# Kernel tuning notes

Hardware: AMD Instinct MI355X
Metric: run time of the kernel (lower is better)

Reference implementation:

```python
import jax, jax.numpy as jnp
import numpy as np

N, E, B = 20000, 320000, 64
HID, DEPTH, NFREQ = 128, 4, 8
NODE_DIM, EDGE_DIM, SG = 4, 3, 230
TWO_PI = 2.0 * np.pi


def setup_inputs() -> dict:
    key = jax.random.key(0)
    ks = jax.random.split(key, 20)
    inp = {}
    inp["x"] = jax.random.normal(ks[0], (N, NODE_DIM), jnp.float32)
    inp["edge_index"] = jax.random.randint(ks[1], (2, E), 0, N)
    inp["edge_attr"] = jax.random.normal(ks[2], (E, EDGE_DIM), jnp.float32)
    inp["batch"] = jnp.sort(jax.random.randint(ks[3], (N,), 0, B))
    inp["space_group"] = jax.random.randint(ks[4], (B,), 0, SG)
    inp["node_w"] = jax.random.normal(ks[5], (NODE_DIM, HID), jnp.float32) * 0.1
    inp["node_b"] = jnp.zeros((HID,), jnp.float32)
    inp["sg_table"] = jax.random.normal(ks[6], (SG, HID), jnp.float32) * 0.1
    inp["lin_w"] = jax.random.normal(ks[7], (DEPTH, 2 * HID + EDGE_DIM, HID), jnp.float32) * 0.05
    inp["lin_b"] = jnp.zeros((DEPTH, HID), jnp.float32)
    inp["att_w"] = jax.random.normal(ks[8], (DEPTH, 2 * HID + EDGE_DIM), jnp.float32) * 0.05
    inp["att_b"] = jnp.zeros((DEPTH,), jnp.float32)
    inp["fk_w"] = jax.random.normal(ks[9], (DEPTH, NFREQ, HID, HID), jnp.float32) * 0.1
    inp["fk_b"] = jnp.zeros((DEPTH, HID), jnp.float32)
    inp["bn_g"] = jnp.ones((DEPTH, HID), jnp.float32)
    inp["bn_b"] = jnp.zeros((DEPTH, HID), jnp.float32)
    inp["pool_w"] = jax.random.normal(ks[10], (HID,), jnp.float32) * 0.1
    inp["pool_b"] = jnp.zeros((), jnp.float32)
    inp["head_w1"] = jax.random.normal(ks[11], (4, 2 * HID, HID), jnp.float32) * 0.05
    inp["head_b1"] = jnp.zeros((4, HID), jnp.float32)
    for i, (nm, od) in enumerate([("e", 1), ("s", 3), ("c", 7), ("m", 3)]):
        inp[nm + "_w2"] = jax.random.normal(ks[12 + i], (HID, od), jnp.float32) * 0.05
        inp[nm + "_b2"] = jnp.zeros((od,), jnp.float32)
    return inp


def reference(x, edge_index, edge_attr, batch, space_group, node_w, node_b, sg_table,
              lin_w, lin_b, att_w, att_b, fk_w, fk_b, bn_g, bn_b, pool_w, pool_b,
              head_w1, head_b1, e_w2, e_b2, s_w2, s_b2, c_w2, c_b2, m_w2, m_b2):
    src, dst = edge_index[0], edge_index[1]  # x_j = x[src], x_i = x[dst]
    h = x @ node_w + node_b                  # [N, HID]
    sg = sg_table[space_group]               # [B, HID]
    freqs = jnp.arange(1, NFREQ + 1, dtype=h.dtype)
    for l in range(DEPTH):
        # edge conv: gather-concat-linear-sigmoid attention-scatter add
        tmp = jnp.concatenate([h[dst], h[src], edge_attr], axis=-1)   # [E, 2H+3]
        alpha = jax.nn.sigmoid(tmp @ att_w[l] + att_b[l])[:, None]    # [E, 1]
        msg = alpha * (tmp @ lin_w[l] + lin_b[l])                     # [E, H]
        h_conv = jax.ops.segment_sum(msg, dst, num_segments=N)
        # Fourier-Kolmogorov branch
        ang = TWO_PI * freqs[None, :, None] * h[:, None, :]           # [N, K, H]
        h_fk = (jnp.einsum('nki,kio->no', jnp.sin(ang), fk_w[l])
                + jnp.einsum('nki,kio->no', jnp.cos(ang), fk_w[l]) + fk_b[l])
        h = h_conv + h_fk
        # BatchNorm1d (batch statistics, training semantics) + ReLU; dropout = identity (eval)
        mu = h.mean(axis=0)
        var = h.var(axis=0)
        h = (h - mu) / jnp.sqrt(var + 1e-5) * bn_g[l] + bn_b[l]
        h = jax.nn.relu(h)
    # attention pool: softmax over ALL nodes (dim=0), as in the original
    a = jax.nn.softmax(h @ pool_w + pool_b, axis=0)[:, None]          # [N, 1]
    pooled = jax.ops.segment_sum(a * h, batch, num_segments=B)        # [B, H]
    comb = jnp.concatenate([pooled, sg], axis=-1)                     # [B, 2H]

    def head(i, w2, b2):
        z = jax.nn.relu(comb @ head_w1[i] + head_b1[i])
        return z @ w2 + b2

    energy = head(0, e_w2, e_b2)          # [B, 1]
    stability = head(1, s_w2, s_b2)       # [B, 3]
    crystal_system = head(2, c_w2, c_b2)  # [B, 7]
    material_type = head(3, m_w2, m_b2)   # [B, 3]
    return energy, stability, crystal_system, material_type
```

## Files before the change

### kernel.cpp

```cpp
#include <hip/hip_runtime.h>
#include <math.h>

#define HID 128
#define DEPTH 4
#define PSPLIT 16
#define SMAXB 40

typedef _Float16 half8 __attribute__((ext_vector_type(8)));
typedef float f4 __attribute__((ext_vector_type(4)));

__global__ void k_node_embed(const float* __restrict__ x, const float* __restrict__ nw,
                             const float* __restrict__ nb, float* __restrict__ h, int N) {
    int idx = blockIdx.x * blockDim.x + threadIdx.x;
    if (idx >= N * HID) return;
    int n = idx >> 7, c = idx & 127;
    float acc = nb[c];
#pragma unroll
    for (int d = 0; d < 4; ++d) acc += x[n * 4 + d] * nw[d * HID + c];
    h[idx] = acc;
}

__global__ void k_wsplit(const float* __restrict__ fkw, _Float16* __restrict__ whi,
                         _Float16* __restrict__ wlo) {
    __shared__ float sh[64][65];
    int bid = blockIdx.x;
    int l = bid >> 5; int r = bid & 31; int kb = r >> 1; int nbk = r & 1;
    const float* W = fkw + (size_t)l * 131072;
    _Float16* Hl = whi + (size_t)l * 131072;
    _Float16* Ll = wlo + (size_t)l * 131072;
    int k0 = kb * 64, n0 = nbk * 64;
    for (int i = threadIdx.x; i < 4096; i += 256) {
        int kk = i >> 6, nn = i & 63;
        sh[kk][nn] = W[(k0 + kk) * HID + n0 + nn];
    }
    __syncthreads();
    for (int i = threadIdx.x; i < 4096; i += 256) {
        int nn = i >> 6, kk = i & 63;
        float w = sh[kk][nn];
        _Float16 hi = (_Float16)w;
        _Float16 lo = (_Float16)((w - (float)hi) * 2048.f);
        Hl[(n0 + nn) * 1024 + k0 + kk] = hi;
        Ll[(n0 + nn) * 1024 + k0 + kk] = lo;
    }
}

__global__ void k_hist(const int* __restrict__ dst, int* __restrict__ deg, int E) {
    int e = blockIdx.x * 256 + threadIdx.x;
    if (e < E) atomicAdd(&deg[dst[e]], 1);
}

__global__ void k_scan_a(const int* __restrict__ deg, int* __restrict__ bsum, int N) {
    __shared__ int sh[256];
    int i = blockIdx.x * 256 + threadIdx.x;
    sh[threadIdx.x] = (i < N) ? deg[i] : 0;
    __syncthreads();
    for (int off = 128; off > 0; off >>= 1) {
        if (threadIdx.x < (unsigned)off) sh[threadIdx.x] += sh[threadIdx.x + off];
        __syncthreads();
    }
    if (threadIdx.x == 0) bsum[blockIdx.x] = sh[0];
}

__global__ void k_scan_b(int* __restrict__ bsum, int nb) {
    __shared__ int sh[256];
    int v = (threadIdx.x < (unsigned)nb) ? bsum[threadIdx.x] : 0;
    sh[threadIdx.x] = v;
    __syncthreads();
    for (int off = 1; off < 256; off <<= 1) {
        int add = (threadIdx.x >= (unsigned)off) ? sh[threadIdx.x - off] : 0;
        __syncthreads();
        sh[threadIdx.x] += add;
        __syncthreads();
    }
    if (threadIdx.x < (unsigned)nb) bsum[threadIdx.x] = sh[threadIdx.x] - v;
}

__global__ void k_scan_c(const int* __restrict__ deg, const int* __restrict__ bsum,
                         int* __restrict__ offs, int* __restrict__ cursor, int N) {
    __shared__ int sh[256];
    int i = blockIdx.x * 256 + threadIdx.x;
    int v = (i < N) ? deg[i] : 0;
    sh[threadIdx.x] = v;
    __syncthreads();
    for (int off = 1; off < 256; off <<= 1) {
        int add = (threadIdx.x >= (unsigned)off) ? sh[threadIdx.x - off] : 0;
        __syncthreads();
        sh[threadIdx.x] += add;
        __syncthreads();
    }
    int ex = bsum[blockIdx.x] + sh[threadIdx.x] - v;
    if (i < N) { offs[i] = ex; cursor[i] = ex; }
    if (i == N - 1) offs[N] = ex + v;
}

__global__ void k_scatter(const int* __restrict__ src, const int* __restrict__ dst,
                          const float* __restrict__ ea, int* cursor,
                          int* __restrict__ srco, float4* __restrict__ ea3o, int E) {
    int e = blockIdx.x * 256 + threadIdx.x;
    if (e < E) {
        int d = dst[e];
        int p = atomicAdd(&cursor[d], 1);
        srco[p] = src[e];
        float4 q;
        q.x = ea[e * 3 + 0]; q.y = ea[e * 3 + 1]; q.z = ea[e * 3 + 2]; q.w = 0.f;
        ea3o[p] = q;
    }
}

__global__ void k_bstart(const int* __restrict__ batch, int* __restrict__ boffs, int N, int B) {
    int n = blockIdx.x * 256 + threadIdx.x;
    if (n >= N) return;
    int b1 = batch[n];
    if (n == 0) for (int b = 0; b <= b1; ++b) boffs[b] = 0;
    int b2 = (n + 1 < N) ? batch[n + 1] : B;
    for (int b = b1 + 1; b <= b2; ++b) boffs[b] = n + 1;
}

__global__ __launch_bounds__(256) void k_node_lin(const float* __restrict__ h,
                           const float* __restrict__ linw, const float* __restrict__ linb,
                           const float* __restrict__ attw, const float* __restrict__ attb,
                           float* __restrict__ A1, float* __restrict__ A2,
                           float* __restrict__ a1, float* __restrict__ a2, int N) {
    __shared__ float hT[HID][20];
    int nb = blockIdx.x * 16;
    int tid = threadIdx.x;
    for (int i = tid; i < 16 * HID; i += 256) {
        int n = i >> 7, c = i & 127;
        int gn = nb + n;
        hT[c][n] = (gn < N) ? h[gn * HID + c] : 0.f;
    }
    __syncthreads();
    {
        int node = tid >> 4, lane16 = tid & 15;
        float p1 = 0.f, p2 = 0.f;
#pragma unroll
        for (int j = 0; j < 8; ++j) {
            int k = lane16 * 8 + j;
            float hv = hT[k][node];
            p1 += hv * attw[k];
            p2 += hv * attw[128 + k];
        }
        for (int off = 8; off > 0; off >>= 1) {
            p1 += __shfl_down(p1, off, 16);
            p2 += __shfl_down(p2, off, 16);
        }
        int gn = nb + node;
        if (lane16 == 0 && gn < N) {
            a1[gn] = p1 + attb[0];
            a2[gn] = p2;
        }
    }
    int c = tid & 127, r = tid >> 7;
    const float* Wd = linw;
    const float* Ws = linw + 128 * HID;
    float acc1[8] = {0, 0, 0, 0, 0, 0, 0, 0}, acc2[8] = {0, 0, 0, 0, 0, 0, 0, 0};
#pragma unroll 4
    for (int k = 0; k < HID; ++k) {
        float wd = Wd[k * HID + c];
        float ws = Ws[k * HID + c];
        float4 h0 = *(const float4*)&hT[k][r * 8];
        float4 h1 = *(const float4*)&hT[k][r * 8 + 4];
        acc1[0] += h0.x * wd; acc2[0] += h0.x * ws;
        acc1[1] += h0.y * wd; acc2[1] += h0.y * ws;
        acc1[2] += h0.z * wd; acc2[2] += h0.z * ws;
        acc1[3] += h0.w * wd; acc2[3] += h0.w * ws;
        acc1[4] += h1.x * wd; acc2[4] += h1.x * ws;
        acc1[5] += h1.y * wd; acc2[5] += h1.y * ws;
        acc1[6] += h1.z * wd; acc2[6] += h1.z * ws;
        acc1[7] += h1.w * wd; acc2[7] += h1.w * ws;
    }
    float lb = linb[c];
#pragma unroll
    for (int j = 0; j < 8; ++j) {
        int gn = nb + r * 8 + j;
        if (gn < N) {
            A1[(size_t)gn * HID + c] = acc1[j] + lb;
            A2[(size_t)gn * HID + c] = acc2[j];
        }
    }
}

__global__ __launch_bounds__(256) void k_edge(const float* __restrict__ A1,
        const float* __restrict__ A2, const float* __restrict__ a1,
        const float* __restrict__ a2, const int* __restrict__ srco,
        const float4* __restrict__ ea3o, const int* __restrict__ offs,
        const float* __restrict__ linw3, const float* __restrict__ attw3,
        float* __restrict__ hconv, double* __restrict__ stats, int N) {
    __shared__ float part[8][HID + 4];
    int n = blockIdx.x;
    int tid = threadIdx.x;
    if (n == 0) stats[tid] = 0.0;
    int lane32 = tid & 31, slot = tid >> 5;
    int c4 = lane32 * 4;
    float4 w0v = *(const float4*)&linw3[c4];
    float4 w1v = *(const float4*)&linw3[HID + c4];
    float4 w2v = *(const float4*)&linw3[2 * HID + c4];
    float aw0 = attw3[0], aw1 = attw3[1], aw2 = attw3[2];
    float a1n = a1[n];
    float4 A1v = *(const float4*)&A1[(size_t)n * HID + c4];
    float4 acc; acc.x = acc.y = acc.z = acc.w = 0.f;
    int s0 = offs[n], s1 = offs[n + 1];
    for (int idx = s0 + slot; idx < s1; idx += 8) {
        int s = srco[idx];
        float4 q = ea3o[idx];
        float logit = a1n + a2[s] + q.x * aw0 + q.y * aw1 + q.z * aw2;
        float al = 1.f / (1.f + __expf(-logit));
        float4 a2v = *(const float4*)&A2[(size_t)s * HID + c4];
        float4 pre;
        pre.x = A1v.x + a2v.x + q.x * w0v.x + q.y * w1v.x + q.z * w2v.x;
        pre.y = A1v.y + a2v.y + q.x * w0v.y + q.y * w1v.y + q.z * w2v.y;
        pre.z = A1v.z + a2v.z + q.x * w0v.z + q.y * w1v.z + q.z * w2v.z;
        pre.w = A1v.w + a2v.w + q.x * w0v.w + q.y * w1v.w + q.z * w2v.w;
        acc.x += al * pre.x; acc.y += al * pre.y;
        acc.z += al * pre.z; acc.w += al * pre.w;
    }
    *(float4*)&part[slot][c4] = acc;
    __syncthreads();
    if (slot == 0) {
        float4 p = *(const float4*)&part[0][c4];
#pragma unroll
        for (int s = 1; s < 8; ++s) {
            float4 r = *(const float4*)&part[s][c4];
            p.x += r.x; p.y += r.y; p.z += r.z; p.w += r.w;
        }
        *(float4*)&hconv[(size_t)n * HID + c4] = p;
    }
}

#define FK_MT 64
__global__ __launch_bounds__(512, 4) void k_fk(const float* __restrict__ h,
        const _Float16* __restrict__ whi, const _Float16* __restrict__ wlo,
        float* __restrict__ p0, float* __restrict__ p1,
        float* __restrict__ p2, float* __restrict__ p3, int N) {
    __shared__ _Float16 ahi[FK_MT * 256];
    __shared__ _Float16 alo[FK_MT * 256];
    int tid = threadIdx.x;
    int bx = blockIdx.x;
    int nb = (bx >> 2) * FK_MT;
    int ks = bx & 3;
    int kbase = ks * 256;
    int fr0 = kbase >> 7;
    {
        int row = tid >> 3;
        int o8 = tid & 7;
        int gn = nb + row;
        int rc = (gn < N) ? gn : (N - 1);
        const float* hp = h + (size_t)rc * HID + o8 * 8;
        float hv[2][8];
        *(float4*)&hv[0][0] = *(const float4*)hp;
        *(float4*)&hv[0][4] = *(const float4*)(hp + 4);
        *(float4*)&hv[1][0] = *(const float4*)(hp + 64);
        *(float4*)&hv[1][4] = *(const float4*)(hp + 68);
        int rs = row & 7;
#pragma unroll
        for (int g = 0; g < 2; ++g) {
            float freqf = 6.2831853f * (float)(fr0 + g + 1);
#pragma unroll
            for (int s = 0; s < 2; ++s) {
                half8 vh, vl;
#pragma unroll
                for (int j = 0; j < 8; ++j) {
                    float ang = freqf * hv[s][j] + 0.78539816f;
                    float a = 1.41421356f * __sinf(ang);
                    _Float16 hi = (_Float16)a;
                    vh[j] = hi;
                    vl[j] = (_Float16)((a - (float)hi) * 2048.f);
                }
                int oct = (g * 16 + s * 8 + o8) ^ rs;
                *(half8*)&ahi[row * 256 + oct * 8] = vh;
                *(half8*)&alo[row * 256 + oct * 8] = vl;
            }
        }
    }
    __syncthreads();
    int lane = tid & 63, wv = tid >> 6;
    int quad = lane >> 4, l16 = lane & 15;
    int n0w = wv * 16;
    f4 acc0[4], accL[4];
#pragma unroll
    for (int mi = 0; mi < 4; ++mi) { acc0[mi] = (f4)(0.f); accL[mi] = (f4)(0.f); }
    const _Float16* bhp = whi + (size_t)(n0w + l16) * 1024 + kbase + quad * 8;
    const _Float16* blp = wlo + (size_t)(n0w + l16) * 1024 + kbase + quad * 8;
    int rs16 = (l16 & 7) << 3;
#pragma unroll 2
    for (int step = 0; step < 8; ++step) {
        int ka = (step * 32 + quad * 8) ^ rs16;
        int ko = step * 32;
        half8 bh = *(const half8*)(bhp + ko);
        half8 bl = *(const half8*)(blp + ko);
        half8 ah[4], al[4];
#pragma unroll
        for (int mi = 0; mi < 4; ++mi) {
            ah[mi] = *(const half8*)&ahi[(l16 + mi * 16) * 256 + ka];
            al[mi] = *(const half8*)&alo[(l16 + mi * 16) * 256 + ka];
        }
#pragma unroll
        for (int mi = 0; mi < 4; ++mi) {
            acc0[mi] = __builtin_amdgcn_mfma_f32_16x16x32_f16(ah[mi], bh, acc0[mi], 0, 0, 0);
            accL[mi] = __builtin_amdgcn_mfma_f32_16x16x32_f16(ah[mi], bl, accL[mi], 0, 0, 0);
            accL[mi] = __builtin_amdgcn_mfma_f32_16x16x32_f16(al[mi], bh, accL[mi], 0, 0, 0);
        }
    }
    float* p = (ks == 0) ? p0 : (ks == 1) ? p1 : (ks == 2) ? p2 : p3;
    const float inv = 1.0f / 2048.0f;
#pragma unroll
    for (int mi = 0; mi < 4; ++mi)
#pragma unroll
        for (int r = 0; r < 4; ++r) {
            int gn = nb + mi * 16 + quad * 4 + r;
            if (gn < N)
                p[gn * HID + n0w + l16] = acc0[mi][r] + accL[mi][r] * inv;
        }
}

__global__ __launch_bounds__(256) void k_bn_stats(float* __restrict__ hconv,
                           const float* __restrict__ p0, const float* __restrict__ p1,
                           const float* __restrict__ p2, const float* __restrict__ p3,
                           const float* __restrict__ fkb,
                           double* __restrict__ stats, int N) {
    int tid = threadIdx.x;
    int cq = tid & 31, rg = tid >> 5;
    int c4 = cq * 4;
    float4 bias = *(const float4*)&fkb[c4];
    float s1[4] = {0, 0, 0, 0}, s2[4] = {0, 0, 0, 0};
    for (int n = blockIdx.x * 8 + rg; n < N; n += gridDim.x * 8) {
        size_t idx = (size_t)n * HID + c4;
        float4 a  = *(const float4*)&hconv[idx];
        float4 b0 = *(const float4*)&p0[idx];
        float4 b1 = *(const float4*)&p1[idx];
        float4 b2 = *(const float4*)&p2[idx];
        float4 b3 = *(const float4*)&p3[idx];
        float4 v;
        v.x = a.x + b0.x + b1.x + b2.x + b3.x + bias.x;
        v.y = a.y + b0.y + b1.y + b2.y + b3.y + bias.y;
        v.z = a.z + b0.z + b1.z + b2.z + b3.z + bias.z;
        v.w = a.w + b0.w + b1.w + b2.w + b3.w + bias.w;
        *(float4*)&hconv[idx] = v;
        s1[0] += v.x; s2[0] += v.x * v.x;
        s1[1] += v.y; s2[1] += v.y * v.y;
        s1[2] += v.z; s2[2] += v.z * v.z;
        s1[3] += v.w; s2[3] += v.w * v.w;
    }
#pragma unroll
    for (int j = 0; j < 4; ++j) {
        s1[j] += __shfl_down(s1[j], 32);
        s2[j] += __shfl_down(s2[j], 32);
    }
    __shared__ float sh1[4][32][4], sh2[4][32][4];
    int wv = tid >> 6, lane = tid & 63;
    if (lane < 32) {
#pragma unroll
        for (int j = 0; j < 4; ++j) { sh1[wv][lane][j] = s1[j]; sh2[wv][lane][j] = s2[j]; }
    }
    __syncthreads();
    if (tid < 128) {
        int cq2 = tid >> 2, j2 = tid & 3;
        float t1 = sh1[0][cq2][j2] + sh1[1][cq2][j2] + sh1[2][cq2][j2] + sh1[3][cq2][j2];
        float t2 = sh2[0][cq2][j2] + sh2[1][cq2][j2] + sh2[2][cq2][j2] + sh2[3][cq2][j2];
        int c = cq2 * 4 + j2;
        atomicAdd(&stats[c], (double)t1);
        atomicAdd(&stats[128 + c], (double)t2);
    }
}

__global__ void k_bn_apply(const float* __restrict__ hsum, const double* __restrict__ stats,
                           const float* __restrict__ g, const float* __restrict__ b,
                           const float* __restrict__ pw, const float* __restrict__ pb,
                           float* __restrict__ h, float* __restrict__ s,
                           int do_score, int N) {
    int idx = blockIdx.x * 256 + threadIdx.x;
    int row = idx >> 5, cq = idx & 31;
    int c4 = cq * 4;
    int valid = row < N;
    double invN = 1.0 / (double)N;
    float p = 0.f;
    if (valid) {
        float4 hv = *(const float4*)&hsum[(size_t)row * HID + c4];
        float vin[4] = {hv.x, hv.y, hv.z, hv.w};
        float4 ov;
        float* po = &ov.x;
#pragma unroll
        for (int j = 0; j < 4; ++j) {
            int c = c4 + j;
            float mu = (float)(stats[c] * invN);
            float var = (float)(stats[128 + c] * invN) - mu * mu;
            float inv = 1.f / sqrtf(var + 1e-5f);
            float sc = g[c] * inv;
            float sh = b[c] - mu * sc;
            float oo = fmaxf(vin[j] * sc + sh, 0.f);
            po[j] = oo;
            if (do_score) p += oo * pw[c];
        }
        *(float4*)&h[(size_t)row * HID + c4] = ov;
    }
    if (do_score) {
        for (int off = 16; off > 0; off >>= 1) p += __shfl_down(p, off, 32);
        if ((threadIdx.x & 31) == 0 && valid) s[row] = p + pb[0];
    }
}

__global__ void k_smax1(const float* __restrict__ s, float* __restrict__ mzp, int N) {
    __shared__ float red[256];
    float m = -INFINITY;
    for (int n = blockIdx.x * 256 + threadIdx.x; n < N; n += SMAXB * 256)
        m = fmaxf(m, s[n]);
    red[threadIdx.x] = m;
    __syncthreads();
    for (int off = 128; off > 0; off >>= 1) {
        if (threadIdx.x < (unsigned)off)
            red[threadIdx.x] = fmaxf(red[threadIdx.x], red[threadIdx.x + off]);
        __syncthreads();
    }
    m = red[0];
    __syncthreads();
    float z = 0.f;
    for (int n = blockIdx.x * 256 + threadIdx.x; n < N; n += SMAXB * 256)
        z += __expf(s[n] - m);
    red[threadIdx.x] = z;
    __syncthreads();
    for (int off = 128; off > 0; off >>= 1) {
        if (threadIdx.x < (unsigned)off) red[threadIdx.x] += red[threadIdx.x + off];
        __syncthreads();
    }
    if (threadIdx.x == 0) { mzp[blockIdx.x * 2] = m; mzp[blockIdx.x * 2 + 1] = red[0]; }
}

__device__ __forceinline__ void combine_mz(const float* mzp, float& m, float& Z) {
    m = -INFINITY;
#pragma unroll 8
    for (int i = 0; i < SMAXB; ++i) m = fmaxf(m, mzp[i * 2]);
    Z = 0.f;
#pragma unroll 8
    for (int i = 0; i < SMAXB; ++i) Z += mzp[i * 2 + 1] * __expf(mzp[i * 2] - m);
}

__global__ void k_pool_part(const float* __restrict__ h, const float* __restrict__ s,
                            const float* __restrict__ mzp, const int* __restrict__ boffs,
                            float* __restrict__ part) {
    int b = blockIdx.x >> 4, split = blockIdx.x & (PSPLIT - 1);
    int c = threadIdx.x & 127, half = threadIdx.x >> 7;
    float m, Z;
    combine_mz(mzp, m, Z);
    (void)Z;
    int n0 = boffs[b], n1 = boffs[b + 1];
    float acc = 0.f;
    for (int n = n0 + split * 2 + half; n < n1; n += PSPLIT * 2)
        acc += __expf(s[n] - m) * h[n * HID + c];
    __shared__ float prt[2][HID];
    prt[half][c] = acc;
    __syncthreads();
    if (half == 0) part[(size_t)(b * PSPLIT + split) * HID + c] = prt[0][c] + prt[1][c];
}

__global__ void k_pool_sum(const float* __restrict__ part, const float* __restrict__ mzp,
                           float* __restrict__ pooled) {
    int b = blockIdx.x, c = threadIdx.x;
    float m, Z;
    combine_mz(mzp, m, Z);
    float acc = 0.f;
#pragma unroll
    for (int i = 0; i < PSPLIT; ++i) acc += part[(size_t)(b * PSPLIT + i) * HID + c];
    pooled[b * HID + c] = acc / Z;
}

__global__ __launch_bounds__(256) void k_head(const float* __restrict__ pooled,
                       const float* __restrict__ sg_table,
                       const int* __restrict__ space_group,
                       const float* __restrict__ hw1, const float* __restrict__ hb1,
                       const float* __restrict__ ew2, const float* __restrict__ eb2,
                       const float* __restrict__ sw2, const float* __restrict__ sb2,
                       const float* __restrict__ cw2, const float* __restrict__ cb2,
                       const float* __restrict__ mw2, const float* __restrict__ mb2,
                       float* __restrict__ out, int B) {
    __shared__ float comb[256];
    __shared__ float zred[2][128];
    __shared__ float zsh[128];
    int b = blockIdx.x >> 2, i = blockIdx.x & 3;
    int t = threadIdx.x;
    comb[t] = (t < 128) ? pooled[b * HID + t] : sg_table[space_group[b] * HID + (t - 128)];
    __syncthreads();
    int half = t >> 7, tt = t & 127;
    const float* W = hw1 + ((size_t)i * 256 + half * 128) * HID;
    const float* cb = &comb[half * 128];
    float z = 0.f;
#pragma unroll 8
    for (int k = 0; k < 128; ++k) z += cb[k] * W[k * HID + tt];
    zred[half][tt] = z;
    __syncthreads();
    if (t < 128) zsh[t] = fmaxf(zred[0][t] + zred[1][t] + hb1[i * HID + t], 0.f);
    __syncthreads();
    const int od[4] = {1, 3, 7, 3};
    const int base[4] = {0, 64, 256, 704};
    const float* w2 = (i == 0) ? ew2 : (i == 1) ? sw2 : (i == 2) ? cw2 : mw2;
    const float* b2 = (i == 0) ? eb2 : (i == 1) ? sb2 : (i == 2) ? cb2 : mb2;
    int odi = od[i];
    if (t < odi) {
        float o = b2[t];
        for (int c = 0; c < HID; ++c) o += zsh[c] * w2[c * odi + t];
        out[base[i] + b * odi + t] = o;
    }
}

extern "C" void kernel_launch(void* const* d_in, const int* in_sizes, int n_in,
                              void* d_out, int out_size, void* d_ws, size_t ws_size,
                              hipStream_t stream) {
    const float* x          = (const float*)d_in[0];
    const int*   edge_index = (const int*)d_in[1];
    const float* edge_attr  = (const float*)d_in[2];
    const int*   batch      = (const int*)d_in[3];
    const int*   space_group= (const int*)d_in[4];
    const float* node_w     = (const float*)d_in[5];
    const float* node_b     = (const float*)d_in[6];
    const float* sg_table   = (const float*)d_in[7];
    const float* lin_w      = (const float*)d_in[8];
    const float* lin_b      = (const float*)d_in[9];
    const float* att_w      = (const float*)d_in[10];
    const float* att_b      = (const float*)d_in[11];
    const float* fk_w       = (const float*)d_in[12];
    const float* fk_b       = (const float*)d_in[13];
    const float* bn_g       = (const float*)d_in[14];
    const float* bn_b       = (const float*)d_in[15];
    const float* pool_w     = (const float*)d_in[16];
    const float* pool_b     = (const float*)d_in[17];
    const float* head_w1    = (const float*)d_in[18];
    const float* head_b1    = (const float*)d_in[19];
    const float* ew2 = (const float*)d_in[20]; const float* eb2 = (const float*)d_in[21];
    const float* sw2 = (const float*)d_in[22]; const float* sb2 = (const float*)d_in[23];
    const float* cw2 = (const float*)d_in[24]; const float* cb2 = (const float*)d_in[25];
    const float* mw2 = (const float*)d_in[26]; const float* mb2 = (const float*)d_in[27];
    float* out = (float*)d_out;

    const int N = in_sizes[3];
    const int E = in_sizes[1] / 2;
    const int B = in_sizes[4];
    const int* src = edge_index;
    const int* dst = edge_index + E;

    char* w = (char*)d_ws;
    auto alloc = [&](size_t bytes) { char* p = w; w += (bytes + 255) & ~(size_t)255; return p; };
    float*  h      = (float*)alloc((size_t)N * HID * 4);
    float*  A1     = (float*)alloc((size_t)N * HID * 4);
    float*  A2     = (float*)alloc((size_t)N * HID * 4);
    float*  p2     = (float*)alloc((size_t)N * HID * 4);
    float*  p3     = (float*)alloc((size_t)N * HID * 4);
    float*  hconv  = (float*)alloc((size_t)N * HID * 4);
    float*  a1     = (float*)alloc((size_t)N * 4);
    float*  a2     = (float*)alloc((size_t)N * 4);
    float*  sbuf   = (float*)alloc((size_t)N * 4);
    int*    deg    = (int*)alloc((size_t)N * 4);
    int*    cursor = (int*)alloc((size_t)N * 4);
    int*    offs   = (int*)alloc((size_t)(N + 1) * 4);
    int*    srco   = (int*)alloc((size_t)E * 4);
    float4* ea3o   = (float4*)alloc((size_t)E * 16);
    _Float16* whi  = (_Float16*)alloc((size_t)DEPTH * 1024 * HID * 2);
    _Float16* wlo  = (_Float16*)alloc((size_t)DEPTH * 1024 * HID * 2);
    int*    bsum   = (int*)alloc(256 * 4);
    int*    boffs  = (int*)alloc((size_t)(B + 1) * 4);
    double* stats  = (double*)alloc(256 * 8);
    float*  mzp    = (float*)alloc(SMAXB * 2 * 4);
    float*  part   = (float*)alloc((size_t)B * PSPLIT * HID * 4);
    float*  pooled = (float*)alloc((size_t)B * HID * 4);

    const int nchunk = (N + 255) / 256;
    const int echunk = (E + 255) / 256;

    k_wsplit<<<128, 256, 0, stream>>>(fk_w, whi, wlo);
    hipMemsetAsync(deg, 0, (size_t)N * 4, stream);
    k_hist<<<echunk, 256, 0, stream>>>(dst, deg, E);
    k_scan_a<<<nchunk, 256, 0, stream>>>(deg, bsum, N);
    k_scan_b<<<1, 256, 0, stream>>>(bsum, nchunk);
    k_scan_c<<<nchunk, 256, 0, stream>>>(deg, bsum, offs, cursor, N);
    k_scatter<<<echunk, 256, 0, stream>>>(src, dst, edge_attr, cursor, srco, ea3o, E);
    k_bstart<<<nchunk, 256, 0, stream>>>(batch, boffs, N, B);

    k_node_embed<<<(N * HID + 255) / 256, 256, 0, stream>>>(x, node_w, node_b, h, N);

    for (int l = 0; l < DEPTH; ++l) {
        const float* linw_l = lin_w + (size_t)l * 259 * HID;
        k_node_lin<<<(N + 15) / 16, 256, 0, stream>>>(
            h, linw_l, lin_b + l * HID, att_w + (size_t)l * 259, att_b + l,
            A1, A2, a1, a2, N);
        k_edge<<<N, 256, 0, stream>>>(A1, A2, a1, a2, srco, ea3o, offs,
                                      linw_l + 256 * HID, att_w + (size_t)l * 259 + 256,
                                      hconv, stats, N);
        k_fk<<<((N + 63) / 64) * 4, 512, 0, stream>>>(
            h, whi + (size_t)l * 131072, wlo + (size_t)l * 131072, A1, A2, p2, p3, N);
        k_bn_stats<<<320, 256, 0, stream>>>(hconv, A1, A2, p2, p3, fk_b + l * HID, stats, N);
        k_bn_apply<<<(N * 32 + 255) / 256, 256, 0, stream>>>(
            hconv, stats, bn_g + l * HID, bn_b + l * HID, pool_w, pool_b,
            h, sbuf, (l == DEPTH - 1) ? 1 : 0, N);
    }

    k_smax1<<<SMAXB, 256, 0, stream>>>(sbuf, mzp, N);
    k_pool_part<<<B * PSPLIT, 256, 0, stream>>>(h, sbuf, mzp, boffs, part);
    k_pool_sum<<<B, 128, 0, stream>>>(part, mzp, pooled);
    k_head<<<B * 4, 256, 0, stream>>>(pooled, sg_table, space_group, head_w1, head_b1,
                                      ew2, eb2, sw2, sb2, cw2, cb2, mw2, mb2, out, B);
}
```

Measured before the change: 668.4 us.

## Restructure Fourier GEMM to 2-way K split with 32-row tiles

The Fourier-kernel GEMM moves from a 4-way K split over 64-row tiles to a 2-way K split over 32-row tiles, each block looping over two K chunks. This halves the partial-sum buffers written by k_fk and read back by k_bn_stats, which cuts global memory traffic and frees two N×128 workspace arrays. In exchange each block does less MFMA work per A-tile load, reloads weight fragments for each chunk, and adds extra __syncthreads around the chunk loop.

```diff
diff --git a/kernel.cpp b/kernel.cpp
--- a/kernel.cpp
+++ b/kernel.cpp
@@ -227,95 +227,93 @@
     }
 }
 
-#define FK_MT 64
+#define FK_ROWS 32
 __global__ __launch_bounds__(512, 4) void k_fk(const float* __restrict__ h,
         const _Float16* __restrict__ whi, const _Float16* __restrict__ wlo,
-        float* __restrict__ p0, float* __restrict__ p1,
-        float* __restrict__ p2, float* __restrict__ p3, int N) {
-    __shared__ _Float16 ahi[FK_MT * 256];
-    __shared__ _Float16 alo[FK_MT * 256];
+        float* __restrict__ p0, float* __restrict__ p1, int N) {
+    __shared__ _Float16 ahi[FK_ROWS * 256];
+    __shared__ _Float16 alo[FK_ROWS * 256];
     int tid = threadIdx.x;
     int bx = blockIdx.x;
-    int nb = (bx >> 2) * FK_MT;
-    int ks = bx & 3;
-    int kbase = ks * 256;
-    int fr0 = kbase >> 7;
+    int nb = (bx >> 1) * FK_ROWS;
+    int ks = bx & 1;
+    int row = tid >> 4;
+    int o16 = tid & 15;
     {
-        int row = tid >> 3;
-        int o8 = tid & 7;
-        int gn = nb + row;
-        int rc = (gn < N) ? gn : (N - 1);
-        const float* hp = h + (size_t)rc * HID + o8 * 8;
-        float hv[2][8];
-        *(float4*)&hv[0][0] = *(const float4*)hp;
-        *(float4*)&hv[0][4] = *(const float4*)(hp + 4);
-        *(float4*)&hv[1][0] = *(const float4*)(hp + 64);
-        *(float4*)&hv[1][4] = *(const float4*)(hp + 68);
-        int rs = row & 7;
-#pragma unroll
-        for (int g = 0; g < 2; ++g) {
-            float freqf = 6.2831853f * (float)(fr0 + g + 1);
-#pragma unroll
-            for (int s = 0; s < 2; ++s) {
-                half8 vh, vl;
-#pragma unroll
-                for (int j = 0; j < 8; ++j) {
-                    float ang = freqf * hv[s][j] + 0.78539816f;
-                    float a = 1.41421356f * __sinf(ang);
-                    _Float16 hi = (_Float16)a;
-                    vh[j] = hi;
-                    vl[j] = (_Float16)((a - (float)hi) * 2048.f);
-                }
-                int oct = (g * 16 + s * 8 + o8) ^ rs;
-                *(half8*)&ahi[row * 256 + oct * 8] = vh;
-                *(half8*)&alo[row * 256 + oct * 8] = vl;
-            }
-        }
-    }
-    __syncthreads();
+    }
+    int gn = nb + row;
+    int rc = (gn < N) ? gn : (N - 1);
+    const float* hp = h + (size_t)rc * HID + o16 * 8;
+    float hv[8];
+    *(float4*)&hv[0] = *(const float4*)hp;
+    *(float4*)&hv[4] = *(const float4*)(hp + 4);
+    int rs = row & 7;
     int lane = tid & 63, wv = tid >> 6;
     int quad = lane >> 4, l16 = lane & 15;
     int n0w = wv * 16;
-    f4 acc0[4], accL[4];
-#pragma unroll
-    for (int mi = 0; mi < 4; ++mi) { acc0[mi] = (f4)(0.f); accL[mi] = (f4)(0.f); }
-    const _Float16* bhp = whi + (size_t)(n0w + l16) * 1024 + kbase + quad * 8;
-    const _Float16* blp = wlo + (size_t)(n0w + l16) * 1024 + kbase + quad * 8;
     int rs16 = (l16 & 7) << 3;
+    f4 acc0[2], accL[2];
+#pragma unroll
+    for (int mi = 0; mi < 2; ++mi) { acc0[mi] = (f4)(0.f); accL[mi] = (f4)(0.f); }
+    int kbase0 = ks * 512;
+#pragma unroll
+    for (int chunk = 0; chunk < 2; ++chunk) {
+        int kbase = kbase0 + chunk * 256;
+        int fr0 = kbase >> 7;
+#pragma unroll
+        for (int g = 0; g < 2; ++g) {
+            float freqf = 6.2831853f * (float)(fr0 + g + 1);
+            half8 vh, vl;
+#pragma unroll
+            for (int j = 0; j < 8; ++j) {
+                float ang = freqf * hv[j] + 0.78539816f;
+                float a = 1.41421356f * __sinf(ang);
+                _Float16 hi = (_Float16)a;
+                vh[j] = hi;
+                vl[j] = (_Float16)((a - (float)hi) * 2048.f);
+            }
+            int oct = (g * 16 + o16) ^ rs;
+            *(half8*)&ahi[row * 256 + oct * 8] = vh;
+            *(half8*)&alo[row * 256 + oct * 8] = vl;
+        }
+        __syncthreads();
+        const _Float16* bhp = whi + (size_t)(n0w + l16) * 1024 + kbase + quad * 8;
+        const _Float16* blp = wlo + (size_t)(n0w + l16) * 1024 + kbase + quad * 8;
 #pragma unroll 2
-    for (int step = 0; step < 8; ++step) {
-        int ka = (step * 32 + quad * 8) ^ rs16;
-        int ko = step * 32;
-        half8 bh = *(const half8*)(bhp + ko);
-        half8 bl = *(const half8*)(blp + ko);
-        half8 ah[4], al[4];
-#pragma unroll
-        for (int mi = 0; mi < 4; ++mi) {
-            ah[mi] = *(const half8*)&ahi[(l16 + mi * 16) * 256 + ka];
-            al[mi] = *(const half8*)&alo[(l16 + mi * 16) * 256 + ka];
-        }
-#pragma unroll
-        for (int mi = 0; mi < 4; ++mi) {
-            acc0[mi] = __builtin_amdgcn_mfma_f32_16x16x32_f16(ah[mi], bh, acc0[mi], 0, 0, 0);
-            accL[mi] = __builtin_amdgcn_mfma_f32_16x16x32_f16(ah[mi], bl, accL[mi], 0, 0, 0);
-            accL[mi] = __builtin_amdgcn_mfma_f32_16x16x32_f16(al[mi], bh, accL[mi], 0, 0, 0);
-        }
-    }
-    float* p = (ks == 0) ? p0 : (ks == 1) ? p1 : (ks == 2) ? p2 : p3;
+        for (int step = 0; step < 8; ++step) {
+            int ka = (step * 32 + quad * 8) ^ rs16;
+            int ko = step * 32;
+            half8 bh = *(const half8*)(bhp + ko);
+            half8 bl = *(const half8*)(blp + ko);
+            half8 ah[2], al[2];
+#pragma unroll
+            for (int mi = 0; mi < 2; ++mi) {
+                ah[mi] = *(const half8*)&ahi[(l16 + mi * 16) * 256 + ka];
+                al[mi] = *(const half8*)&alo[(l16 + mi * 16) * 256 + ka];
+            }
+#pragma unroll
+            for (int mi = 0; mi < 2; ++mi) {
+                acc0[mi] = __builtin_amdgcn_mfma_f32_16x16x32_f16(ah[mi], bh, acc0[mi], 0, 0, 0);
+                accL[mi] = __builtin_amdgcn_mfma_f32_16x16x32_f16(ah[mi], bl, accL[mi], 0, 0, 0);
+                accL[mi] = __builtin_amdgcn_mfma_f32_16x16x32_f16(al[mi], bh, accL[mi], 0, 0, 0);
+            }
+        }
+        __syncthreads();
+    }
+    float* p = ks ? p1 : p0;
     const float inv = 1.0f / 2048.0f;
 #pragma unroll
-    for (int mi = 0; mi < 4; ++mi)
+    for (int mi = 0; mi < 2; ++mi)
 #pragma unroll
         for (int r = 0; r < 4; ++r) {
-            int gn = nb + mi * 16 + quad * 4 + r;
-            if (gn < N)
-                p[gn * HID + n0w + l16] = acc0[mi][r] + accL[mi][r] * inv;
+            int g2 = nb + mi * 16 + quad * 4 + r;
+            if (g2 < N)
+                p[g2 * HID + n0w + l16] = acc0[mi][r] + accL[mi][r] * inv;
         }
 }
 
 __global__ __launch_bounds__(256) void k_bn_stats(float* __restrict__ hconv,
                            const float* __restrict__ p0, const float* __restrict__ p1,
-                           const float* __restrict__ p2, const float* __restrict__ p3,
                            const float* __restrict__ fkb,
                            double* __restrict__ stats, int N) {
     int tid = threadIdx.x;
@@ -328,13 +326,11 @@
         float4 a  = *(const float4*)&hconv[idx];
         float4 b0 = *(const float4*)&p0[idx];
         float4 b1 = *(const float4*)&p1[idx];
-        float4 b2 = *(const float4*)&p2[idx];
-        float4 b3 = *(const float4*)&p3[idx];
         float4 v;
-        v.x = a.x + b0.x + b1.x + b2.x + b3.x + bias.x;
-        v.y = a.y + b0.y + b1.y + b2.y + b3.y + bias.y;
-        v.z = a.z + b0.z + b1.z + b2.z + b3.z + bias.z;
-        v.w = a.w + b0.w + b1.w + b2.w + b3.w + bias.w;
+        v.x = a.x + b0.x + b1.x + bias.x;
+        v.y = a.y + b0.y + b1.y + bias.y;
+        v.z = a.z + b0.z + b1.z + bias.z;
+        v.w = a.w + b0.w + b1.w + bias.w;
         *(float4*)&hconv[idx] = v;
         s1[0] += v.x; s2[0] += v.x * v.x;
         s1[1] += v.y; s2[1] += v.y * v.y;
@@ -541,8 +537,6 @@
     float*  h      = (float*)alloc((size_t)N * HID * 4);
     float*  A1     = (float*)alloc((size_t)N * HID * 4);
     float*  A2     = (float*)alloc((size_t)N * HID * 4);
-    float*  p2     = (float*)alloc((size_t)N * HID * 4);
-    float*  p3     = (float*)alloc((size_t)N * HID * 4);
     float*  hconv  = (float*)alloc((size_t)N * HID * 4);
     float*  a1     = (float*)alloc((size_t)N * 4);
     float*  a2     = (float*)alloc((size_t)N * 4);
@@ -583,9 +577,9 @@
         k_edge<<<N, 256, 0, stream>>>(A1, A2, a1, a2, srco, ea3o, offs,
                                       linw_l + 256 * HID, att_w + (size_t)l * 259 + 256,
                                       hconv, stats, N);
-        k_fk<<<((N + 63) / 64) * 4, 512, 0, stream>>>(
-            h, whi + (size_t)l * 131072, wlo + (size_t)l * 131072, A1, A2, p2, p3, N);
-        k_bn_stats<<<320, 256, 0, stream>>>(hconv, A1, A2, p2, p3, fk_b + l * HID, stats, N);
+        k_fk<<<((N + FK_ROWS - 1) / FK_ROWS) * 2, 512, 0, stream>>>(
+            h, whi + (size_t)l * 131072, wlo + (size_t)l * 131072, A1, A2, N);
+        k_bn_stats<<<320, 256, 0, stream>>>(hconv, A1, A2, fk_b + l * HID, stats, N);
         k_bn_apply<<<(N * 32 + 255) / 256, 256, 0, stream>>>(
             hconv, stats, bn_g + l * HID, bn_b + l * HID, pool_w, pool_b,
             h, sbuf, (l == DEPTH - 1) ? 1 : 0, N);
```

New measurement: 709.8 us. +6.2%, slower.

## Move node linear projection onto split-fp16 MFMA GEMM with pre-split weights

Applied to the files above, without the earlier changes.

Replaces the scalar FP32 node_lin kernel, which computed the A1/A2 projections, with an MFMA-based GEMM. Each FP32 operand is split into fp16 hi and scaled lo parts, and three MFMA products are combined to keep accuracy close to FP32. A new setup kernel pre-transposes and splits the lin_w weights once. Activations are staged in XOR-swizzled LDS tiles to avoid bank conflicts. The goal is to cut the per-layer FMA cost of this projection, in exchange for a small precision change and extra weight storage.

```diff
diff --git a/kernel.cpp b/kernel.cpp
--- a/kernel.cpp
+++ b/kernel.cpp
@@ -44,6 +44,31 @@
     }
 }
 
+__global__ void k_wsplit2(const float* __restrict__ linw, _Float16* __restrict__ lwhi,
+                          _Float16* __restrict__ lwlo) {
+    __shared__ float sh[64][65];
+    int bid = blockIdx.x;
+    int l = bid >> 3; int r = bid & 7; int cb = r >> 1; int kb = r & 1;
+    const float* W = linw + (size_t)l * 259 * HID;
+    int c0 = cb * 64, k0 = kb * 64;
+    const float* base = W + (size_t)((c0 >= 128) ? 128 : 0) * HID + (c0 & 127);
+    for (int i = threadIdx.x; i < 4096; i += 256) {
+        int kk = i >> 6, cc = i & 63;
+        sh[kk][cc] = base[(size_t)(k0 + kk) * HID + cc];
+    }
+    __syncthreads();
+    _Float16* Hl = lwhi + (size_t)l * 32768;
+    _Float16* Ll = lwlo + (size_t)l * 32768;
+    for (int i = threadIdx.x; i < 4096; i += 256) {
+        int cc = i >> 6, kk = i & 63;
+        float w = sh[kk][cc];
+        _Float16 hi = (_Float16)w;
+        _Float16 lo = (_Float16)((w - (float)hi) * 2048.f);
+        Hl[(size_t)(c0 + cc) * 128 + k0 + kk] = hi;
+        Ll[(size_t)(c0 + cc) * 128 + k0 + kk] = lo;
+    }
+}
+
 __global__ void k_hist(const int* __restrict__ dst, int* __restrict__ deg, int E) {
     int e = blockIdx.x * 256 + threadIdx.x;
     if (e < E) atomicAdd(&deg[dst[e]], 1);
@@ -116,68 +141,105 @@
     for (int b = b1 + 1; b <= b2; ++b) boffs[b] = n + 1;
 }
 
-__global__ __launch_bounds__(256) void k_node_lin(const float* __restrict__ h,
-                           const float* __restrict__ linw, const float* __restrict__ linb,
-                           const float* __restrict__ attw, const float* __restrict__ attb,
-                           float* __restrict__ A1, float* __restrict__ A2,
-                           float* __restrict__ a1, float* __restrict__ a2, int N) {
-    __shared__ float hT[HID][20];
-    int nb = blockIdx.x * 16;
+__global__ __launch_bounds__(512, 4) void k_nlgemm(const float* __restrict__ h,
+        const _Float16* __restrict__ lwhi, const _Float16* __restrict__ lwlo,
+        const float* __restrict__ linb,
+        const float* __restrict__ attw, const float* __restrict__ attb,
+        float* __restrict__ A1, float* __restrict__ A2,
+        float* __restrict__ a1, float* __restrict__ a2, int N) {
+    __shared__ _Float16 ahi[32 * 128];
+    __shared__ _Float16 alo[32 * 128];
     int tid = threadIdx.x;
-    for (int i = tid; i < 16 * HID; i += 256) {
-        int n = i >> 7, c = i & 127;
-        int gn = nb + n;
-        hT[c][n] = (gn < N) ? h[gn * HID + c] : 0.f;
-    }
-    __syncthreads();
+    int nb = blockIdx.x * 32;
     {
-        int node = tid >> 4, lane16 = tid & 15;
+        int row = tid >> 4;
+        int o16 = tid & 15;
+        int gn = nb + row;
+        int rc = (gn < N) ? gn : (N - 1);
+        const float* hp = h + (size_t)rc * HID + o16 * 8;
+        float hv[8];
+        *(float4*)&hv[0] = *(const float4*)hp;
+        *(float4*)&hv[4] = *(const float4*)(hp + 4);
         float p1 = 0.f, p2 = 0.f;
 #pragma unroll
         for (int j = 0; j < 8; ++j) {
-            int k = lane16 * 8 + j;
-            float hv = hT[k][node];
-            p1 += hv * attw[k];
-            p2 += hv * attw[128 + k];
+            int k = o16 * 8 + j;
+            p1 += hv[j] * attw[k];
+            p2 += hv[j] * attw[128 + k];
         }
         for (int off = 8; off > 0; off >>= 1) {
             p1 += __shfl_down(p1, off, 16);
             p2 += __shfl_down(p2, off, 16);
         }
-        int gn = nb + node;
-        if (lane16 == 0 && gn < N) {
+        if (o16 == 0 && gn < N) {
             a1[gn] = p1 + attb[0];
             a2[gn] = p2;
         }
-    }
-    int c = tid & 127, r = tid >> 7;
-    const float* Wd = linw;
-    const float* Ws = linw + 128 * HID;
-    float acc1[8] = {0, 0, 0, 0, 0, 0, 0, 0}, acc2[8] = {0, 0, 0, 0, 0, 0, 0, 0};
-#pragma unroll 4
-    for (int k = 0; k < HID; ++k) {
-        float wd = Wd[k * HID + c];
-        float ws = Ws[k * HID + c];
-        float4 h0 = *(const float4*)&hT[k][r * 8];
-        float4 h1 = *(const float4*)&hT[k][r * 8 + 4];
-        acc1[0] += h0.x * wd; acc2[0] += h0.x * ws;
-        acc1[1] += h0.y * wd; acc2[1] += h0.y * ws;
-        acc1[2] += h0.z * wd; acc2[2] += h0.z * ws;
-        acc1[3] += h0.w * wd; acc2[3] += h0.w * ws;
-        acc1[4] += h1.x * wd; acc2[4] += h1.x * ws;
-        acc1[5] += h1.y * wd; acc2[5] += h1.y * ws;
-        acc1[6] += h1.z * wd; acc2[6] += h1.z * ws;
-        acc1[7] += h1.w * wd; acc2[7] += h1.w * ws;
-    }
-    float lb = linb[c];
-#pragma unroll
-    for (int j = 0; j < 8; ++j) {
-        int gn = nb + r * 8 + j;
-        if (gn < N) {
-            A1[(size_t)gn * HID + c] = acc1[j] + lb;
-            A2[(size_t)gn * HID + c] = acc2[j];
-        }
-    }
+        int rs = row & 7;
+        half8 vh, vl;
+#pragma unroll
+        for (int j = 0; j < 8; ++j) {
+            float a = hv[j];
+            _Float16 hi = (_Float16)a;
+            vh[j] = hi;
+            vl[j] = (_Float16)((a - (float)hi) * 2048.f);
+        }
+        int oct = o16 ^ rs;
+        *(half8*)&ahi[row * 128 + oct * 8] = vh;
+        *(half8*)&alo[row * 128 + oct * 8] = vl;
+    }
+    __syncthreads();
+    int lane = tid & 63, wv = tid >> 6;
+    int quad = lane >> 4, l16 = lane & 15;
+    int n0 = wv * 32;
+    f4 acc0[2][2], accL[2][2];
+#pragma unroll
+    for (int mi = 0; mi < 2; ++mi)
+#pragma unroll
+        for (int ni = 0; ni < 2; ++ni) { acc0[mi][ni] = (f4)(0.f); accL[mi][ni] = (f4)(0.f); }
+    const _Float16* bhp0 = lwhi + (size_t)(n0 + l16) * 128 + quad * 8;
+    const _Float16* bhp1 = lwhi + (size_t)(n0 + 16 + l16) * 128 + quad * 8;
+    const _Float16* blp0 = lwlo + (size_t)(n0 + l16) * 128 + quad * 8;
+    const _Float16* blp1 = lwlo + (size_t)(n0 + 16 + l16) * 128 + quad * 8;
+    int rs16 = (l16 & 7) << 3;
+#pragma unroll
+    for (int step = 0; step < 4; ++step) {
+        int ka = (step * 32 + quad * 8) ^ rs16;
+        int ko = step * 32;
+        half8 bh0 = *(const half8*)(bhp0 + ko);
+        half8 bh1 = *(const half8*)(bhp1 + ko);
+        half8 bl0 = *(const half8*)(blp0 + ko);
+        half8 bl1 = *(const half8*)(blp1 + ko);
+        half8 ah[2], al[2];
+#pragma unroll
+        for (int mi = 0; mi < 2; ++mi) {
+            ah[mi] = *(const half8*)&ahi[(l16 + mi * 16) * 128 + ka];
+            al[mi] = *(const half8*)&alo[(l16 + mi * 16) * 128 + ka];
+        }
+#pragma unroll
+        for (int mi = 0; mi < 2; ++mi) {
+            acc0[mi][0] = __builtin_amdgcn_mfma_f32_16x16x32_f16(ah[mi], bh0, acc0[mi][0], 0, 0, 0);
+            acc0[mi][1] = __builtin_amdgcn_mfma_f32_16x16x32_f16(ah[mi], bh1, acc0[mi][1], 0, 0, 0);
+            accL[mi][0] = __builtin_amdgcn_mfma_f32_16x16x32_f16(ah[mi], bl0, accL[mi][0], 0, 0, 0);
+            accL[mi][1] = __builtin_amdgcn_mfma_f32_16x16x32_f16(ah[mi], bl1, accL[mi][1], 0, 0, 0);
+            accL[mi][0] = __builtin_amdgcn_mfma_f32_16x16x32_f16(al[mi], bh0, accL[mi][0], 0, 0, 0);
+            accL[mi][1] = __builtin_amdgcn_mfma_f32_16x16x32_f16(al[mi], bh1, accL[mi][1], 0, 0, 0);
+        }
+    }
+    const float inv = 1.0f / 2048.0f;
+#pragma unroll
+    for (int mi = 0; mi < 2; ++mi)
+#pragma unroll
+        for (int ni = 0; ni < 2; ++ni)
+#pragma unroll
+            for (int r = 0; r < 4; ++r) {
+                int gn = nb + mi * 16 + quad * 4 + r;
+                if (gn >= N) continue;
+                int cp = n0 + ni * 16 + l16;
+                float val = acc0[mi][ni][r] + accL[mi][ni][r] * inv;
+                if (cp < 128) A1[(size_t)gn * HID + cp] = val + linb[cp];
+                else          A2[(size_t)gn * HID + cp - 128] = val;
+            }
 }
 
 __global__ __launch_bounds__(256) void k_edge(const float* __restrict__ A1,
@@ -554,6 +616,8 @@
     float4* ea3o   = (float4*)alloc((size_t)E * 16);
     _Float16* whi  = (_Float16*)alloc((size_t)DEPTH * 1024 * HID * 2);
     _Float16* wlo  = (_Float16*)alloc((size_t)DEPTH * 1024 * HID * 2);
+    _Float16* lwhi = (_Float16*)alloc((size_t)DEPTH * 256 * HID * 2);
+    _Float16* lwlo = (_Float16*)alloc((size_t)DEPTH * 256 * HID * 2);
     int*    bsum   = (int*)alloc(256 * 4);
     int*    boffs  = (int*)alloc((size_t)(B + 1) * 4);
     double* stats  = (double*)alloc(256 * 8);
@@ -565,6 +629,7 @@
     const int echunk = (E + 255) / 256;
 
     k_wsplit<<<128, 256, 0, stream>>>(fk_w, whi, wlo);
+    k_wsplit2<<<32, 256, 0, stream>>>(lin_w, lwhi, lwlo);
     hipMemsetAsync(deg, 0, (size_t)N * 4, stream);
     k_hist<<<echunk, 256, 0, stream>>>(dst, deg, E);
     k_scan_a<<<nchunk, 256, 0, stream>>>(deg, bsum, N);
@@ -577,13 +642,14 @@
 
     for (int l = 0; l < DEPTH; ++l) {
         const float* linw_l = lin_w + (size_t)l * 259 * HID;
-        k_node_lin<<<(N + 15) / 16, 256, 0, stream>>>(
-            h, linw_l, lin_b + l * HID, att_w + (size_t)l * 259, att_b + l,
+        k_nlgemm<<<(N + 31) / 32, 512, 0, stream>>>(
+            h, lwhi + (size_t)l * 32768, lwlo + (size_t)l * 32768,
+            lin_b + l * HID, att_w + (size_t)l * 259, att_b + l,
             A1, A2, a1, a2, N);
         k_edge<<<N, 256, 0, stream>>>(A1, A2, a1, a2, srco, ea3o, offs,
                                       linw_l + 256 * HID, att_w + (size_t)l * 259 + 256,
                                       hconv, stats, N);
-        k_fk<<<((N + 63) / 64) * 4, 512, 0, stream>>>(
+        k_fk<<<((N + FK_MT - 1) / FK_MT) * 4, 512, 0, stream>>>(
             h, whi + (size_t)l * 131072, wlo + (size_t)l * 131072, A1, A2, p2, p3, N);
         k_bn_stats<<<320, 256, 0, stream>>>(hconv, A1, A2, p2, p3, fk_b + l * HID, stats, N);
         k_bn_apply<<<(N * 32 + 255) / 256, 256, 0, stream>>>(
```

New measurement: 645.8 us. 3.4% less time.
